# Kernel optimization log

Hardware: AMD Instinct MI355X
Metric: run time of the kernel (lower is better)

Reference implementation:

```python
import jax, jax.numpy as jnp
import numpy as np

SEQ_LEN = 4096
D_IN = 1024
D_OUT = 1024


def setup_inputs() -> dict:
    key = jax.random.key(0)
    k_x, k_q, k_k, k_v = jax.random.split(key, 4)
    s = 1.0 / np.sqrt(D_IN)
    return {
        "x": jax.random.normal(k_x, (SEQ_LEN, D_IN), dtype=jnp.float32),
        "W_query": jax.random.normal(k_q, (D_IN, D_OUT), dtype=jnp.float32) * s,
        "W_key": jax.random.normal(k_k, (D_IN, D_OUT), dtype=jnp.float32) * s,
        "W_value": jax.random.normal(k_v, (D_IN, D_OUT), dtype=jnp.float32) * s,
    }


def reference(x, W_query, W_key, W_value):
    # QKV projections (Linear without bias): [S, d_out]
    q = x @ W_query
    k = x @ W_key
    v = x @ W_value
    # Full S x S score matrix, causal mask, scaled softmax
    scores = q @ k.T  # [S, S]
    seq_len = x.shape[0]
    causal = jnp.tril(jnp.ones((seq_len, seq_len), dtype=bool))
    scores = jnp.where(causal, scores, -jnp.inf)
    scale = 1.0 / jnp.sqrt(jnp.asarray(k.shape[-1], dtype=scores.dtype))
    attn = jax.nn.softmax(scores * scale, axis=-1)
    return attn @ v  # [S, d_out]
```

## Files before the change

### kernel.cpp

```cpp
#include <hip/hip_runtime.h>
#include <math.h>

#define SEQ 4096
#define DIM 1024

typedef unsigned short u16;
typedef __attribute__((ext_vector_type(8))) short short8;
typedef __attribute__((ext_vector_type(4))) float floatx4;
typedef __attribute__((ext_vector_type(4))) unsigned short us4;

__device__ __forceinline__ float bf2f(u16 u) {
    union { unsigned int i; float f; } c; c.i = ((unsigned int)u) << 16; return c.f;
}
__device__ __forceinline__ u16 f2bf(float f) {
    union { float f; unsigned int i; } c; c.f = f;
    return (u16)((c.i + 0x7fffu + ((c.i >> 16) & 1u)) >> 16);
}
__device__ __forceinline__ void gload_lds16(const u16* g, u16* l) {
    __builtin_amdgcn_global_load_lds((const __attribute__((address_space(1))) void*)g,
                                     (__attribute__((address_space(3))) void*)l, 16, 0, 0);
}

__device__ __forceinline__ void pipe128(const u16* __restrict__ A,
                                        const u16* __restrict__ B,
                                        u16 (&As)[3][4096], u16 (&Bs)[3][4096],
                                        int lda, int ldb, int row0, int col0,
                                        int wave, int lane,
                                        floatx4 (&acc)[4][4]) {
    const int wm = wave & 1, wn = wave >> 1;
    const int s0 = wave * 128 + lane;
    const int s1 = s0 + 64;
    const int r0s = s0 >> 2, q0s = ((s0 & 3) ^ ((s0 >> 3) & 3)) * 8;
    const int r1s = s1 >> 2, q1s = ((s1 & 3) ^ ((s1 >> 3) & 3)) * 8;
    const u16* aP0 = A + (size_t)(row0 + r0s) * lda + q0s;
    const u16* aP1 = A + (size_t)(row0 + r1s) * lda + q1s;
    const u16* bP0 = B + (size_t)(col0 + r0s) * ldb + q0s;
    const u16* bP1 = B + (size_t)(col0 + r1s) * ldb + q1s;
    const int l0 = wave * 1024;
    const int frow = lane & 15;
    const int xq = (((lane >> 4) ^ ((frow >> 1) & 3))) * 8;

    auto stage = [&](int c) {
        gload_lds16(aP0, &As[c][l0]);
        gload_lds16(aP1, &As[c][l0 + 512]);
        gload_lds16(bP0, &Bs[c][l0]);
        gload_lds16(bP1, &Bs[c][l0 + 512]);
        aP0 += 32; aP1 += 32; bP0 += 32; bP1 += 32;
    };
    stage(0);
    stage(1);

    auto compute_tile = [&](int c) {
        short8 af[4], bfr[4];
#pragma unroll
        for (int t = 0; t < 4; ++t) {
            af[t]  = *(const short8*)&As[c][(wm * 64 + t * 16 + frow) * 32 + xq];
            bfr[t] = *(const short8*)&Bs[c][(wn * 64 + t * 16 + frow) * 32 + xq];
        }
#pragma unroll
        for (int mt = 0; mt < 4; ++mt)
#pragma unroll
            for (int nt = 0; nt < 4; ++nt)
                acc[mt][nt] = __builtin_amdgcn_mfma_f32_16x16x32_bf16(
                    af[mt], bfr[nt], acc[mt][nt], 0, 0, 0);
    };

    int cur = 0, pre = 2;
    for (int it = 0; it < 30; ++it) {
        asm volatile("s_waitcnt vmcnt(4)\n\ts_barrier" ::: "memory");
        short8 af[4], bfr[4];
#pragma unroll
        for (int t = 0; t < 4; ++t) {
            af[t]  = *(const short8*)&As[cur][(wm * 64 + t * 16 + frow) * 32 + xq];
            bfr[t] = *(const short8*)&Bs[cur][(wn * 64 + t * 16 + frow) * 32 + xq];
        }
        stage(pre);
#pragma unroll
        for (int mt = 0; mt < 4; ++mt)
#pragma unroll
            for (int nt = 0; nt < 4; ++nt)
                acc[mt][nt] = __builtin_amdgcn_mfma_f32_16x16x32_bf16(
                    af[mt], bfr[nt], acc[mt][nt], 0, 0, 0);
        cur = (cur == 2) ? 0 : cur + 1;
        pre = (pre == 2) ? 0 : pre + 1;
    }
    asm volatile("s_waitcnt vmcnt(4)\n\ts_barrier" ::: "memory");
    compute_tile(cur);
    cur = (cur == 2) ? 0 : cur + 1;
    asm volatile("s_waitcnt vmcnt(0)\n\ts_barrier" ::: "memory");
    compute_tile(cur);
}

__global__ __launch_bounds__(256) void projQK(const u16* __restrict__ xb,
                                              const u16* __restrict__ Wt,
                                              u16* __restrict__ QK,
                                              float scale0) {
    __shared__ u16 As[3][4096], Bs[3][4096];
    const int row0 = blockIdx.y * 128;
    const int col0 = blockIdx.x * 128;
    const int tid = threadIdx.x, wave = tid >> 6, lane = tid & 63;
    const int wm = wave & 1, wn = wave >> 1;

    floatx4 acc[4][4] = {};
    pipe128(xb, Wt, As, Bs, DIM, DIM, row0, col0, wave, lane, acc);

    const int cr = (lane >> 4) * 4, cc = lane & 15;
    const float sc = (col0 < 1024) ? scale0 : 1.0f;
#pragma unroll
    for (int mt = 0; mt < 4; ++mt)
#pragma unroll
        for (int nt = 0; nt < 4; ++nt)
#pragma unroll
            for (int r = 0; r < 4; ++r) {
                const int row = row0 + wm * 64 + mt * 16 + cr + r;
                const int col = col0 + wn * 64 + nt * 16 + cc;
                QK[(size_t)row * 2048 + col] = f2bf(acc[mt][nt][r] * sc);
            }
}

__global__ __launch_bounds__(256) void scoresV(const u16* __restrict__ QK,
                                               const u16* __restrict__ xb,
                                               const u16* __restrict__ Wt,
                                               u16* __restrict__ E,
                                               u16* __restrict__ Vt,
                                               float* __restrict__ Lsum) {
    __shared__ u16 As[3][4096], Bs[3][4096];
    const int t = blockIdx.x;
    const int tid = threadIdx.x, wave = tid >> 6, lane = tid & 63;
    const int wm = wave & 1, wn = wave >> 1;
    const int cr = (lane >> 4) * 4, cc = lane & 15;

    floatx4 acc[4][4] = {};
    if (t < 256) {
        const int row0 = (t >> 3) * 128;
        const int colv = (t & 7) * 128;
        pipe128(xb, Wt, As, Bs, DIM, DIM, row0, 2048 + colv, wave, lane, acc);
#pragma unroll
        for (int mt = 0; mt < 4; ++mt)
#pragma unroll
            for (int nt = 0; nt < 4; ++nt) {
                const int row = row0 + wm * 64 + mt * 16 + cr;
                const int col = colv + wn * 64 + nt * 16 + cc;
                us4 o = { f2bf(acc[mt][nt][0]), f2bf(acc[mt][nt][1]),
                          f2bf(acc[mt][nt][2]), f2bf(acc[mt][nt][3]) };
                *(us4*)&Vt[(size_t)col * SEQ + row] = o;
            }
    } else {
        const int s = t - 256;
        int by = (int)((sqrtf(8.0f * s + 1.0f) - 1.0f) * 0.5f);
        while ((by + 1) * (by + 2) / 2 <= s) ++by;
        while (by * (by + 1) / 2 > s) --by;
        const int bx = s - by * (by + 1) / 2;
        const int row0 = by * 128, col0 = bx * 128;
        pipe128(QK, QK + 1024, As, Bs, 2048, 2048, row0, col0, wave, lane, acc);
#pragma unroll
        for (int mt = 0; mt < 4; ++mt) {
#pragma unroll
            for (int r = 0; r < 4; ++r) {
                const int grow = row0 + wm * 64 + mt * 16 + cr + r;
                float rowsum = 0.f;
#pragma unroll
                for (int nt = 0; nt < 4; ++nt) {
                    const int gcol = col0 + wn * 64 + nt * 16 + cc;
                    const float e = (gcol <= grow) ? __expf(acc[mt][nt][r]) : 0.f;
                    rowsum += e;
                    E[(size_t)grow * SEQ + gcol] = f2bf(e);
                }
                rowsum += __shfl_xor(rowsum, 1);
                rowsum += __shfl_xor(rowsum, 2);
                rowsum += __shfl_xor(rowsum, 4);
                rowsum += __shfl_xor(rowsum, 8);
                if (cc == 0) atomicAdd(&Lsum[grow], rowsum);
            }
        }
    }
}

__global__ __launch_bounds__(256) void pv64(const u16* __restrict__ E,
                                            const u16* __restrict__ Vt,
                                            float* __restrict__ O,
                                            const float* __restrict__ Lsum) {
    const int lin = blockIdx.x + (blockIdx.y << 4);
    const int c = lin & 7;
    const int j = lin >> 3;
    const int x = j & 15;
    const int m = j >> 4;
    const unsigned long long PK = 0x2F3F20301F0F1000ULL;
    const int base = (int)((PK >> (m * 8)) & 0x3F);
    const int r = base + ((m & 2) ? -c : c);
    const int row0 = r * 64;
    const int col0 = x * 64;
    const int kend = row0 + 64;

    __shared__ u16 As[3][2048], Bs[3][2048];

    const int tid  = threadIdx.x;
    const int wave = tid >> 6;
    const int lane = tid & 63;
    const int wm = wave & 1;
    const int wn = wave >> 1;

    const int s0 = wave * 64 + lane;
    const int r0 = s0 >> 2, q0 = ((s0 & 3) ^ ((s0 >> 3) & 3)) * 8;
    const u16* aP = E  + (size_t)(row0 + r0) * SEQ + q0;
    const u16* bP = Vt + (size_t)(col0 + r0) * SEQ + q0;
    const int l0 = wave * 512;

    floatx4 acc[2][2] = {};
    const int niter = kend >> 5;
    const int frow = lane & 15;
    const int xq = (((lane >> 4) ^ ((frow >> 1) & 3))) * 8;
    const int mrow0 = wm * 32, nrow0 = wn * 32;

    auto stage = [&](int cb) {
        gload_lds16(aP, &As[cb][l0]);
        gload_lds16(bP, &Bs[cb][l0]);
        aP += 32; bP += 32;
    };
    stage(0);
    stage(1);

    auto compute_tile = [&](int cb) {
        short8 af[2], bfr[2];
#pragma unroll
        for (int t = 0; t < 2; ++t) {
            af[t]  = *(const short8*)&As[cb][(mrow0 + t * 16 + frow) * 32 + xq];
            bfr[t] = *(const short8*)&Bs[cb][(nrow0 + t * 16 + frow) * 32 + xq];
        }
#pragma unroll
        for (int mt = 0; mt < 2; ++mt)
#pragma unroll
            for (int nt = 0; nt < 2; ++nt)
                acc[mt][nt] = __builtin_amdgcn_mfma_f32_16x16x32_bf16(
                    af[mt], bfr[nt], acc[mt][nt], 0, 0, 0);
    };

    int cur = 0, pre = 2;
    for (int it = 0; it < niter - 2; ++it) {
        asm volatile("s_waitcnt vmcnt(2)\n\ts_barrier" ::: "memory");
        short8 af[2], bfr[2];
#pragma unroll
        for (int t = 0; t < 2; ++t) {
            af[t]  = *(const short8*)&As[cur][(mrow0 + t * 16 + frow) * 32 + xq];
            bfr[t] = *(const short8*)&Bs[cur][(nrow0 + t * 16 + frow) * 32 + xq];
        }
        stage(pre);
#pragma unroll
        for (int mt = 0; mt < 2; ++mt)
#pragma unroll
            for (int nt = 0; nt < 2; ++nt)
                acc[mt][nt] = __builtin_amdgcn_mfma_f32_16x16x32_bf16(
                    af[mt], bfr[nt], acc[mt][nt], 0, 0, 0);
        cur = (cur == 2) ? 0 : cur + 1;
        pre = (pre == 2) ? 0 : pre + 1;
    }
    asm volatile("s_waitcnt vmcnt(2)\n\ts_barrier" ::: "memory");
    compute_tile(cur);
    cur = (cur == 2) ? 0 : cur + 1;
    asm volatile("s_waitcnt vmcnt(0)\n\ts_barrier" ::: "memory");
    compute_tile(cur);

    float* Oo = O;
    const int cr = (lane >> 4) * 4, cc = lane & 15;
#pragma unroll
    for (int mt = 0; mt < 2; ++mt)
#pragma unroll
        for (int rr = 0; rr < 4; ++rr) {
            const int grow = row0 + wm * 32 + mt * 16 + cr + rr;
            const float invl = __builtin_amdgcn_rcpf(Lsum[grow]);
#pragma unroll
            for (int nt = 0; nt < 2; ++nt) {
                const int col = col0 + wn * 32 + nt * 16 + cc;
                Oo[(size_t)grow * DIM + col] = acc[mt][nt][rr] * invl;
            }
        }
}

__global__ __launch_bounds__(256) void prep(const float* __restrict__ x,
                                            const float* __restrict__ W0,
                                            const float* __restrict__ W1,
                                            const float* __restrict__ W2,
                                            u16* __restrict__ xb,
                                            u16* __restrict__ Wt,
                                            float* __restrict__ Lsum) {
    __shared__ float tile[32][33];
    const int b = blockIdx.x;
    const int tid = threadIdx.x;
    if (b < 4096) {
        const size_t i = ((size_t)b * 256 + tid) * 4;
        const float4 v = *(const float4*)(x + i);
        us4 o = { f2bf(v.x), f2bf(v.y), f2bf(v.z), f2bf(v.w) };
        *(us4*)(xb + i) = o;
    } else if (b < 7168) {
        const int t = b - 4096;
        const int z = t >> 10;
        const int idx = t & 1023;
        const float* W = (z == 0) ? W0 : (z == 1) ? W1 : W2;
        u16* out = Wt + (size_t)z * DIM * DIM;
        const int bx = (idx & 31) * 32;
        const int by = (idx >> 5) * 32;
        const int tx = tid & 31;
        const int ty = (tid >> 5) * 4;
#pragma unroll
        for (int r = 0; r < 4; ++r)
            tile[ty + r][tx] = W[(size_t)(by + ty + r) * DIM + bx + tx];
        __syncthreads();
#pragma unroll
        for (int r = 0; r < 4; ++r)
            out[(size_t)(bx + ty + r) * DIM + by + tx] = f2bf(tile[tx][ty + r]);
    } else {
        const int t = b - 7168;
        *(float4*)(Lsum + (size_t)(t * 256 + tid) * 4) =
            make_float4(0.f, 0.f, 0.f, 0.f);
    }
}

extern "C" void kernel_launch(void* const* d_in, const int* in_sizes, int n_in,
                              void* d_out, int out_size, void* d_ws, size_t ws_size,
                              hipStream_t stream) {
    const float* x  = (const float*)d_in[0];
    const float* Wq = (const float*)d_in[1];
    const float* Wk = (const float*)d_in[2];
    const float* Wv = (const float*)d_in[3];

    u16* xb    = (u16*)d_ws;
    u16* Wt    = xb  + (size_t)SEQ * DIM;
    u16* QK    = Wt  + (size_t)3072 * DIM;
    u16* Vt    = QK  + (size_t)SEQ * 2048;
    u16* E     = Vt  + (size_t)DIM * SEQ;
    float* Lsum = (float*)(E + (size_t)SEQ * SEQ);

    prep<<<7172, 256, 0, stream>>>(x, Wq, Wk, Wv, xb, Wt, Lsum);

    projQK<<<dim3(16, 32), 256, 0, stream>>>(xb, Wt, QK, 0.03125f);

    scoresV<<<784, 256, 0, stream>>>(QK, xb, Wt, E, Vt, Lsum);

    pv64<<<dim3(16, 64), 256, 0, stream>>>(E, Vt, (float*)d_out, Lsum);
}
```

Before: 192.2 us.

## Switch GEMM pipelines to double-buffered LDS and fold V projection into QK GEMM

The shared pipeline and the PV kernel now use two LDS buffers instead of three. Each iteration adds an lgkmcnt wait and a barrier, then issues the next prefetch into the buffer that was just read. The V projection moves out of the scores kernel into a single QKV projection launch, and scores becomes its own causal-tile kernel. The smaller LDS footprint may raise occupancy and give a more even grid split, but the extra barrier per k-step can expose load latency.

```diff
diff --git a/kernel.cpp b/kernel.cpp
--- a/kernel.cpp
+++ b/kernel.cpp
@@ -23,7 +23,7 @@
 
 __device__ __forceinline__ void pipe128(const u16* __restrict__ A,
                                         const u16* __restrict__ B,
-                                        u16 (&As)[3][4096], u16 (&Bs)[3][4096],
+                                        u16 (&As)[2][4096], u16 (&Bs)[2][4096],
                                         int lda, int ldb, int row0, int col0,
                                         int wave, int lane,
                                         floatx4 (&acc)[4][4]) {
@@ -50,52 +50,53 @@
     stage(0);
     stage(1);
 
-    auto compute_tile = [&](int c) {
+    int cur = 0;
+    for (int it = 0; it < 30; ++it) {
+        asm volatile("s_waitcnt vmcnt(4)\n\ts_barrier" ::: "memory");
         short8 af[4], bfr[4];
 #pragma unroll
         for (int t = 0; t < 4; ++t) {
-            af[t]  = *(const short8*)&As[c][(wm * 64 + t * 16 + frow) * 32 + xq];
-            bfr[t] = *(const short8*)&Bs[c][(wn * 64 + t * 16 + frow) * 32 + xq];
-        }
+            af[t]  = *(const short8*)&As[cur][(wm * 64 + t * 16 + frow) * 32 + xq];
+            bfr[t] = *(const short8*)&Bs[cur][(wn * 64 + t * 16 + frow) * 32 + xq];
+        }
+        asm volatile("s_waitcnt lgkmcnt(0)\n\ts_barrier" ::: "memory");
+        stage(cur);
 #pragma unroll
         for (int mt = 0; mt < 4; ++mt)
 #pragma unroll
             for (int nt = 0; nt < 4; ++nt)
                 acc[mt][nt] = __builtin_amdgcn_mfma_f32_16x16x32_bf16(
                     af[mt], bfr[nt], acc[mt][nt], 0, 0, 0);
-    };
-
-    int cur = 0, pre = 2;
-    for (int it = 0; it < 30; ++it) {
-        asm volatile("s_waitcnt vmcnt(4)\n\ts_barrier" ::: "memory");
+        cur ^= 1;
+    }
+#pragma unroll
+    for (int fin = 0; fin < 2; ++fin) {
+        if (fin == 0)
+            asm volatile("s_waitcnt vmcnt(4)\n\ts_barrier" ::: "memory");
+        else
+            asm volatile("s_waitcnt vmcnt(0)\n\ts_barrier" ::: "memory");
         short8 af[4], bfr[4];
 #pragma unroll
         for (int t = 0; t < 4; ++t) {
             af[t]  = *(const short8*)&As[cur][(wm * 64 + t * 16 + frow) * 32 + xq];
             bfr[t] = *(const short8*)&Bs[cur][(wn * 64 + t * 16 + frow) * 32 + xq];
         }
-        stage(pre);
 #pragma unroll
         for (int mt = 0; mt < 4; ++mt)
 #pragma unroll
             for (int nt = 0; nt < 4; ++nt)
                 acc[mt][nt] = __builtin_amdgcn_mfma_f32_16x16x32_bf16(
                     af[mt], bfr[nt], acc[mt][nt], 0, 0, 0);
-        cur = (cur == 2) ? 0 : cur + 1;
-        pre = (pre == 2) ? 0 : pre + 1;
-    }
-    asm volatile("s_waitcnt vmcnt(4)\n\ts_barrier" ::: "memory");
-    compute_tile(cur);
-    cur = (cur == 2) ? 0 : cur + 1;
-    asm volatile("s_waitcnt vmcnt(0)\n\ts_barrier" ::: "memory");
-    compute_tile(cur);
-}
-
-__global__ __launch_bounds__(256) void projQK(const u16* __restrict__ xb,
-                                              const u16* __restrict__ Wt,
-                                              u16* __restrict__ QK,
-                                              float scale0) {
-    __shared__ u16 As[3][4096], Bs[3][4096];
+        cur ^= 1;
+    }
+}
+
+__global__ __launch_bounds__(256) void gemm128(const u16* __restrict__ xb,
+                                               const u16* __restrict__ Wt,
+                                               u16* __restrict__ QK,
+                                               u16* __restrict__ Vt,
+                                               float scale0) {
+    __shared__ u16 As[2][4096], Bs[2][4096];
     const int row0 = blockIdx.y * 128;
     const int col0 = blockIdx.x * 128;
     const int tid = threadIdx.x, wave = tid >> 6, lane = tid & 63;
@@ -105,73 +106,67 @@
     pipe128(xb, Wt, As, Bs, DIM, DIM, row0, col0, wave, lane, acc);
 
     const int cr = (lane >> 4) * 4, cc = lane & 15;
-    const float sc = (col0 < 1024) ? scale0 : 1.0f;
-#pragma unroll
-    for (int mt = 0; mt < 4; ++mt)
-#pragma unroll
-        for (int nt = 0; nt < 4; ++nt)
-#pragma unroll
-            for (int r = 0; r < 4; ++r) {
-                const int row = row0 + wm * 64 + mt * 16 + cr + r;
-                const int col = col0 + wn * 64 + nt * 16 + cc;
-                QK[(size_t)row * 2048 + col] = f2bf(acc[mt][nt][r] * sc);
-            }
-}
-
-__global__ __launch_bounds__(256) void scoresV(const u16* __restrict__ QK,
-                                               const u16* __restrict__ xb,
-                                               const u16* __restrict__ Wt,
-                                               u16* __restrict__ E,
-                                               u16* __restrict__ Vt,
-                                               float* __restrict__ Lsum) {
-    __shared__ u16 As[3][4096], Bs[3][4096];
-    const int t = blockIdx.x;
-    const int tid = threadIdx.x, wave = tid >> 6, lane = tid & 63;
-    const int wm = wave & 1, wn = wave >> 1;
-    const int cr = (lane >> 4) * 4, cc = lane & 15;
-
-    floatx4 acc[4][4] = {};
-    if (t < 256) {
-        const int row0 = (t >> 3) * 128;
-        const int colv = (t & 7) * 128;
-        pipe128(xb, Wt, As, Bs, DIM, DIM, row0, 2048 + colv, wave, lane, acc);
+    if (col0 >= 2048) {
 #pragma unroll
         for (int mt = 0; mt < 4; ++mt)
 #pragma unroll
             for (int nt = 0; nt < 4; ++nt) {
                 const int row = row0 + wm * 64 + mt * 16 + cr;
-                const int col = colv + wn * 64 + nt * 16 + cc;
+                const int col = (col0 - 2048) + wn * 64 + nt * 16 + cc;
                 us4 o = { f2bf(acc[mt][nt][0]), f2bf(acc[mt][nt][1]),
                           f2bf(acc[mt][nt][2]), f2bf(acc[mt][nt][3]) };
                 *(us4*)&Vt[(size_t)col * SEQ + row] = o;
             }
     } else {
-        const int s = t - 256;
-        int by = (int)((sqrtf(8.0f * s + 1.0f) - 1.0f) * 0.5f);
-        while ((by + 1) * (by + 2) / 2 <= s) ++by;
-        while (by * (by + 1) / 2 > s) --by;
-        const int bx = s - by * (by + 1) / 2;
-        const int row0 = by * 128, col0 = bx * 128;
-        pipe128(QK, QK + 1024, As, Bs, 2048, 2048, row0, col0, wave, lane, acc);
-#pragma unroll
-        for (int mt = 0; mt < 4; ++mt) {
-#pragma unroll
-            for (int r = 0; r < 4; ++r) {
-                const int grow = row0 + wm * 64 + mt * 16 + cr + r;
-                float rowsum = 0.f;
-#pragma unroll
-                for (int nt = 0; nt < 4; ++nt) {
-                    const int gcol = col0 + wn * 64 + nt * 16 + cc;
-                    const float e = (gcol <= grow) ? __expf(acc[mt][nt][r]) : 0.f;
-                    rowsum += e;
-                    E[(size_t)grow * SEQ + gcol] = f2bf(e);
+        const float sc = (col0 < 1024) ? scale0 : 1.0f;
+#pragma unroll
+        for (int mt = 0; mt < 4; ++mt)
+#pragma unroll
+            for (int nt = 0; nt < 4; ++nt)
+#pragma unroll
+                for (int r = 0; r < 4; ++r) {
+                    const int row = row0 + wm * 64 + mt * 16 + cr + r;
+                    const int col = col0 + wn * 64 + nt * 16 + cc;
+                    QK[(size_t)row * 2048 + col] = f2bf(acc[mt][nt][r] * sc);
                 }
-                rowsum += __shfl_xor(rowsum, 1);
-                rowsum += __shfl_xor(rowsum, 2);
-                rowsum += __shfl_xor(rowsum, 4);
-                rowsum += __shfl_xor(rowsum, 8);
-                if (cc == 0) atomicAdd(&Lsum[grow], rowsum);
+    }
+}
+
+__global__ __launch_bounds__(256) void scores(const u16* __restrict__ QK,
+                                              u16* __restrict__ E,
+                                              float* __restrict__ Lsum) {
+    __shared__ u16 As[2][4096], Bs[2][4096];
+    const int t = blockIdx.x;
+    int by = (int)((sqrtf(8.0f * t + 1.0f) - 1.0f) * 0.5f);
+    while ((by + 1) * (by + 2) / 2 <= t) ++by;
+    while (by * (by + 1) / 2 > t) --by;
+    const int bx = t - by * (by + 1) / 2;
+    const int row0 = by * 128, col0 = bx * 128;
+    const int tid = threadIdx.x, wave = tid >> 6, lane = tid & 63;
+    const int wm = wave & 1, wn = wave >> 1;
+
+    floatx4 acc[4][4] = {};
+    pipe128(QK, QK + 1024, As, Bs, 2048, 2048, row0, col0, wave, lane, acc);
+
+    const int cr = (lane >> 4) * 4, cc = lane & 15;
+#pragma unroll
+    for (int mt = 0; mt < 4; ++mt) {
+#pragma unroll
+        for (int r = 0; r < 4; ++r) {
+            const int grow = row0 + wm * 64 + mt * 16 + cr + r;
+            float rowsum = 0.f;
+#pragma unroll
+            for (int nt = 0; nt < 4; ++nt) {
+                const int gcol = col0 + wn * 64 + nt * 16 + cc;
+                const float e = (gcol <= grow) ? __expf(acc[mt][nt][r]) : 0.f;
+                rowsum += e;
+                E[(size_t)grow * SEQ + gcol] = f2bf(e);
             }
+            rowsum += __shfl_xor(rowsum, 1);
+            rowsum += __shfl_xor(rowsum, 2);
+            rowsum += __shfl_xor(rowsum, 4);
+            rowsum += __shfl_xor(rowsum, 8);
+            if (cc == 0) atomicAdd(&Lsum[grow], rowsum);
         }
     }
 }
@@ -192,7 +187,7 @@
     const int col0 = x * 64;
     const int kend = row0 + 64;
 
-    __shared__ u16 As[3][2048], Bs[3][2048];
+    __shared__ u16 As[2][2048], Bs[2][2048];
 
     const int tid  = threadIdx.x;
     const int wave = tid >> 6;
@@ -220,47 +215,46 @@
     stage(0);
     stage(1);
 
-    auto compute_tile = [&](int cb) {
+    int cur = 0;
+    for (int it = 0; it < niter - 2; ++it) {
+        asm volatile("s_waitcnt vmcnt(2)\n\ts_barrier" ::: "memory");
         short8 af[2], bfr[2];
 #pragma unroll
         for (int t = 0; t < 2; ++t) {
-            af[t]  = *(const short8*)&As[cb][(mrow0 + t * 16 + frow) * 32 + xq];
-            bfr[t] = *(const short8*)&Bs[cb][(nrow0 + t * 16 + frow) * 32 + xq];
-        }
+            af[t]  = *(const short8*)&As[cur][(mrow0 + t * 16 + frow) * 32 + xq];
+            bfr[t] = *(const short8*)&Bs[cur][(nrow0 + t * 16 + frow) * 32 + xq];
+        }
+        asm volatile("s_waitcnt lgkmcnt(0)\n\ts_barrier" ::: "memory");
+        stage(cur);
 #pragma unroll
         for (int mt = 0; mt < 2; ++mt)
 #pragma unroll
             for (int nt = 0; nt < 2; ++nt)
                 acc[mt][nt] = __builtin_amdgcn_mfma_f32_16x16x32_bf16(
                     af[mt], bfr[nt], acc[mt][nt], 0, 0, 0);
-    };
-
-    int cur = 0, pre = 2;
-    for (int it = 0; it < niter - 2; ++it) {
-        asm volatile("s_waitcnt vmcnt(2)\n\ts_barrier" ::: "memory");
+        cur ^= 1;
+    }
+#pragma unroll
+    for (int fin = 0; fin < 2; ++fin) {
+        if (fin == 0)
+            asm volatile("s_waitcnt vmcnt(2)\n\ts_barrier" ::: "memory");
+        else
+            asm volatile("s_waitcnt vmcnt(0)\n\ts_barrier" ::: "memory");
         short8 af[2], bfr[2];
 #pragma unroll
         for (int t = 0; t < 2; ++t) {
             af[t]  = *(const short8*)&As[cur][(mrow0 + t * 16 + frow) * 32 + xq];
             bfr[t] = *(const short8*)&Bs[cur][(nrow0 + t * 16 + frow) * 32 + xq];
         }
-        stage(pre);
 #pragma unroll
         for (int mt = 0; mt < 2; ++mt)
 #pragma unroll
             for (int nt = 0; nt < 2; ++nt)
                 acc[mt][nt] = __builtin_amdgcn_mfma_f32_16x16x32_bf16(
                     af[mt], bfr[nt], acc[mt][nt], 0, 0, 0);
-        cur = (cur == 2) ? 0 : cur + 1;
-        pre = (pre == 2) ? 0 : pre + 1;
-    }
-    asm volatile("s_waitcnt vmcnt(2)\n\ts_barrier" ::: "memory");
-    compute_tile(cur);
-    cur = (cur == 2) ? 0 : cur + 1;
-    asm volatile("s_waitcnt vmcnt(0)\n\ts_barrier" ::: "memory");
-    compute_tile(cur);
-
-    float* Oo = O;
+        cur ^= 1;
+    }
+
     const int cr = (lane >> 4) * 4, cc = lane & 15;
 #pragma unroll
     for (int mt = 0; mt < 2; ++mt)
@@ -271,7 +265,7 @@
 #pragma unroll
             for (int nt = 0; nt < 2; ++nt) {
                 const int col = col0 + wn * 32 + nt * 16 + cc;
-                Oo[(size_t)grow * DIM + col] = acc[mt][nt][rr] * invl;
+                O[(size_t)grow * DIM + col] = acc[mt][nt][rr] * invl;
             }
         }
 }
@@ -332,9 +326,9 @@
 
     prep<<<7172, 256, 0, stream>>>(x, Wq, Wk, Wv, xb, Wt, Lsum);
 
-    projQK<<<dim3(16, 32), 256, 0, stream>>>(xb, Wt, QK, 0.03125f);
-
-    scoresV<<<784, 256, 0, stream>>>(QK, xb, Wt, E, Vt, Lsum);
+    gemm128<<<dim3(24, 32), 256, 0, stream>>>(xb, Wt, QK, Vt, 0.03125f);
+
+    scores<<<528, 256, 0, stream>>>(QK, E, Lsum);
 
     pv64<<<dim3(16, 64), 256, 0, stream>>>(E, Vt, (float*)d_out, Lsum);
 }
```

New measurement: 209.8 us. 1.09x slower.

## Use 256x128 tiles with 512 threads and move V projection into projection kernel

Applied to the files above, without the earlier changes.

Replaces the 128x128, 256-thread GEMM pipeline with a 256x128 tile handled by 8 waves and a double-buffered loop that uses __syncthreads instead of a triple-buffered vmcnt pipeline. The V projection moves out of the scores kernel into a single projection launch covering Q, K and V. The scores launch now enumerates 272 causal 256x128 blocks. Larger tiles increase operand reuse per block but cut the number of blocks and the depth of prefetch, which may leave compute units idle or expose load latency.

```diff
diff --git a/kernel.cpp b/kernel.cpp
--- a/kernel.cpp
+++ b/kernel.cpp
@@ -21,41 +21,43 @@
                                      (__attribute__((address_space(3))) void*)l, 16, 0, 0);
 }
 
-__device__ __forceinline__ void pipe128(const u16* __restrict__ A,
+__device__ __forceinline__ void pipe256(const u16* __restrict__ A,
                                         const u16* __restrict__ B,
-                                        u16 (&As)[3][4096], u16 (&Bs)[3][4096],
+                                        u16 (&As)[2][8192], u16 (&Bs)[2][4096],
                                         int lda, int ldb, int row0, int col0,
                                         int wave, int lane,
                                         floatx4 (&acc)[4][4]) {
-    const int wm = wave & 1, wn = wave >> 1;
-    const int s0 = wave * 128 + lane;
-    const int s1 = s0 + 64;
-    const int r0s = s0 >> 2, q0s = ((s0 & 3) ^ ((s0 >> 3) & 3)) * 8;
-    const int r1s = s1 >> 2, q1s = ((s1 & 3) ^ ((s1 >> 3) & 3)) * 8;
-    const u16* aP0 = A + (size_t)(row0 + r0s) * lda + q0s;
-    const u16* aP1 = A + (size_t)(row0 + r1s) * lda + q1s;
-    const u16* bP0 = B + (size_t)(col0 + r0s) * ldb + q0s;
-    const u16* bP1 = B + (size_t)(col0 + r1s) * ldb + q1s;
-    const int l0 = wave * 1024;
+    const int wm = wave & 3, wn = wave >> 2;
+    const int sa0 = wave * 128 + lane, sa1 = sa0 + 64;
+    const int ra0 = sa0 >> 2, qa0 = ((sa0 & 3) ^ ((sa0 >> 3) & 3)) * 8;
+    const int ra1 = sa1 >> 2, qa1 = ((sa1 & 3) ^ ((sa1 >> 3) & 3)) * 8;
+    const int sb0 = wave * 64 + lane;
+    const int rb0 = sb0 >> 2, qb0 = ((sb0 & 3) ^ ((sb0 >> 3) & 3)) * 8;
+    const u16* aP0 = A + (size_t)(row0 + ra0) * lda + qa0;
+    const u16* aP1 = A + (size_t)(row0 + ra1) * lda + qa1;
+    const u16* bP0 = B + (size_t)(col0 + rb0) * ldb + qb0;
+    const int lA = wave * 1024;
+    const int lB = wave * 512;
     const int frow = lane & 15;
     const int xq = (((lane >> 4) ^ ((frow >> 1) & 3))) * 8;
 
     auto stage = [&](int c) {
-        gload_lds16(aP0, &As[c][l0]);
-        gload_lds16(aP1, &As[c][l0 + 512]);
-        gload_lds16(bP0, &Bs[c][l0]);
-        gload_lds16(bP1, &Bs[c][l0 + 512]);
-        aP0 += 32; aP1 += 32; bP0 += 32; bP1 += 32;
+        gload_lds16(aP0, &As[c][lA]);
+        gload_lds16(aP1, &As[c][lA + 512]);
+        gload_lds16(bP0, &Bs[c][lB]);
+        aP0 += 32; aP1 += 32; bP0 += 32;
     };
+
     stage(0);
-    stage(1);
-
-    auto compute_tile = [&](int c) {
+    __syncthreads();
+    for (int it = 0; it < 32; ++it) {
+        const int cur = it & 1;
+        if (it < 31) stage(cur ^ 1);
         short8 af[4], bfr[4];
 #pragma unroll
         for (int t = 0; t < 4; ++t) {
-            af[t]  = *(const short8*)&As[c][(wm * 64 + t * 16 + frow) * 32 + xq];
-            bfr[t] = *(const short8*)&Bs[c][(wn * 64 + t * 16 + frow) * 32 + xq];
+            af[t]  = *(const short8*)&As[cur][(wm * 64 + t * 16 + frow) * 32 + xq];
+            bfr[t] = *(const short8*)&Bs[cur][(wn * 64 + t * 16 + frow) * 32 + xq];
         }
 #pragma unroll
         for (int mt = 0; mt < 4; ++mt)
@@ -63,115 +65,86 @@
             for (int nt = 0; nt < 4; ++nt)
                 acc[mt][nt] = __builtin_amdgcn_mfma_f32_16x16x32_bf16(
                     af[mt], bfr[nt], acc[mt][nt], 0, 0, 0);
-    };
-
-    int cur = 0, pre = 2;
-    for (int it = 0; it < 30; ++it) {
-        asm volatile("s_waitcnt vmcnt(4)\n\ts_barrier" ::: "memory");
-        short8 af[4], bfr[4];
-#pragma unroll
-        for (int t = 0; t < 4; ++t) {
-            af[t]  = *(const short8*)&As[cur][(wm * 64 + t * 16 + frow) * 32 + xq];
-            bfr[t] = *(const short8*)&Bs[cur][(wn * 64 + t * 16 + frow) * 32 + xq];
-        }
-        stage(pre);
-#pragma unroll
-        for (int mt = 0; mt < 4; ++mt)
-#pragma unroll
-            for (int nt = 0; nt < 4; ++nt)
-                acc[mt][nt] = __builtin_amdgcn_mfma_f32_16x16x32_bf16(
-                    af[mt], bfr[nt], acc[mt][nt], 0, 0, 0);
-        cur = (cur == 2) ? 0 : cur + 1;
-        pre = (pre == 2) ? 0 : pre + 1;
-    }
-    asm volatile("s_waitcnt vmcnt(4)\n\ts_barrier" ::: "memory");
-    compute_tile(cur);
-    cur = (cur == 2) ? 0 : cur + 1;
-    asm volatile("s_waitcnt vmcnt(0)\n\ts_barrier" ::: "memory");
-    compute_tile(cur);
-}
-
-__global__ __launch_bounds__(256) void projQK(const u16* __restrict__ xb,
-                                              const u16* __restrict__ Wt,
-                                              u16* __restrict__ QK,
-                                              float scale0) {
-    __shared__ u16 As[3][4096], Bs[3][4096];
-    const int row0 = blockIdx.y * 128;
+        __syncthreads();
+    }
+}
+
+__global__ __launch_bounds__(512) void proj256(const u16* __restrict__ xb,
+                                               const u16* __restrict__ Wt,
+                                               u16* __restrict__ QK,
+                                               u16* __restrict__ Vt,
+                                               float scale0) {
+    __shared__ u16 As[2][8192], Bs[2][4096];
+    const int row0 = blockIdx.y * 256;
     const int col0 = blockIdx.x * 128;
     const int tid = threadIdx.x, wave = tid >> 6, lane = tid & 63;
-    const int wm = wave & 1, wn = wave >> 1;
+    const int wm = wave & 3, wn = wave >> 2;
 
     floatx4 acc[4][4] = {};
-    pipe128(xb, Wt, As, Bs, DIM, DIM, row0, col0, wave, lane, acc);
+    pipe256(xb, Wt, As, Bs, DIM, DIM, row0, col0, wave, lane, acc);
 
     const int cr = (lane >> 4) * 4, cc = lane & 15;
-    const float sc = (col0 < 1024) ? scale0 : 1.0f;
-#pragma unroll
-    for (int mt = 0; mt < 4; ++mt)
-#pragma unroll
-        for (int nt = 0; nt < 4; ++nt)
-#pragma unroll
-            for (int r = 0; r < 4; ++r) {
-                const int row = row0 + wm * 64 + mt * 16 + cr + r;
-                const int col = col0 + wn * 64 + nt * 16 + cc;
-                QK[(size_t)row * 2048 + col] = f2bf(acc[mt][nt][r] * sc);
-            }
-}
-
-__global__ __launch_bounds__(256) void scoresV(const u16* __restrict__ QK,
-                                               const u16* __restrict__ xb,
-                                               const u16* __restrict__ Wt,
-                                               u16* __restrict__ E,
-                                               u16* __restrict__ Vt,
-                                               float* __restrict__ Lsum) {
-    __shared__ u16 As[3][4096], Bs[3][4096];
-    const int t = blockIdx.x;
-    const int tid = threadIdx.x, wave = tid >> 6, lane = tid & 63;
-    const int wm = wave & 1, wn = wave >> 1;
-    const int cr = (lane >> 4) * 4, cc = lane & 15;
-
-    floatx4 acc[4][4] = {};
-    if (t < 256) {
-        const int row0 = (t >> 3) * 128;
-        const int colv = (t & 7) * 128;
-        pipe128(xb, Wt, As, Bs, DIM, DIM, row0, 2048 + colv, wave, lane, acc);
+    if (col0 >= 2048) {
 #pragma unroll
         for (int mt = 0; mt < 4; ++mt)
 #pragma unroll
             for (int nt = 0; nt < 4; ++nt) {
                 const int row = row0 + wm * 64 + mt * 16 + cr;
-                const int col = colv + wn * 64 + nt * 16 + cc;
+                const int col = (col0 - 2048) + wn * 64 + nt * 16 + cc;
                 us4 o = { f2bf(acc[mt][nt][0]), f2bf(acc[mt][nt][1]),
                           f2bf(acc[mt][nt][2]), f2bf(acc[mt][nt][3]) };
                 *(us4*)&Vt[(size_t)col * SEQ + row] = o;
             }
     } else {
-        const int s = t - 256;
-        int by = (int)((sqrtf(8.0f * s + 1.0f) - 1.0f) * 0.5f);
-        while ((by + 1) * (by + 2) / 2 <= s) ++by;
-        while (by * (by + 1) / 2 > s) --by;
-        const int bx = s - by * (by + 1) / 2;
-        const int row0 = by * 128, col0 = bx * 128;
-        pipe128(QK, QK + 1024, As, Bs, 2048, 2048, row0, col0, wave, lane, acc);
-#pragma unroll
-        for (int mt = 0; mt < 4; ++mt) {
-#pragma unroll
-            for (int r = 0; r < 4; ++r) {
-                const int grow = row0 + wm * 64 + mt * 16 + cr + r;
-                float rowsum = 0.f;
-#pragma unroll
-                for (int nt = 0; nt < 4; ++nt) {
-                    const int gcol = col0 + wn * 64 + nt * 16 + cc;
-                    const float e = (gcol <= grow) ? __expf(acc[mt][nt][r]) : 0.f;
-                    rowsum += e;
-                    E[(size_t)grow * SEQ + gcol] = f2bf(e);
+        const float sc = (col0 < 1024) ? scale0 : 1.0f;
+#pragma unroll
+        for (int mt = 0; mt < 4; ++mt)
+#pragma unroll
+            for (int nt = 0; nt < 4; ++nt)
+#pragma unroll
+                for (int r = 0; r < 4; ++r) {
+                    const int row = row0 + wm * 64 + mt * 16 + cr + r;
+                    const int col = col0 + wn * 64 + nt * 16 + cc;
+                    QK[(size_t)row * 2048 + col] = f2bf(acc[mt][nt][r] * sc);
                 }
-                rowsum += __shfl_xor(rowsum, 1);
-                rowsum += __shfl_xor(rowsum, 2);
-                rowsum += __shfl_xor(rowsum, 4);
-                rowsum += __shfl_xor(rowsum, 8);
-                if (cc == 0) atomicAdd(&Lsum[grow], rowsum);
+    }
+}
+
+__global__ __launch_bounds__(512) void scores256(const u16* __restrict__ QK,
+                                                 u16* __restrict__ E,
+                                                 float* __restrict__ Lsum) {
+    __shared__ u16 As[2][8192], Bs[2][4096];
+    const int t = blockIdx.x;
+    int R = (int)((sqrtf(4.0f * t + 1.0f) - 1.0f) * 0.5f);
+    while ((R + 1) * (R + 2) + R + 1 - 1 < t + 1) ++R;
+    while (R * R + R > t) --R;
+    const int bx = t - (R * R + R);
+    const int row0 = R * 256, col0 = bx * 128;
+    const int tid = threadIdx.x, wave = tid >> 6, lane = tid & 63;
+    const int wm = wave & 3, wn = wave >> 2;
+
+    floatx4 acc[4][4] = {};
+    pipe256(QK, QK + 1024, As, Bs, 2048, 2048, row0, col0, wave, lane, acc);
+
+    const int cr = (lane >> 4) * 4, cc = lane & 15;
+#pragma unroll
+    for (int mt = 0; mt < 4; ++mt) {
+#pragma unroll
+        for (int r = 0; r < 4; ++r) {
+            const int grow = row0 + wm * 64 + mt * 16 + cr + r;
+            float rowsum = 0.f;
+#pragma unroll
+            for (int nt = 0; nt < 4; ++nt) {
+                const int gcol = col0 + wn * 64 + nt * 16 + cc;
+                const float e = (gcol <= grow) ? __expf(acc[mt][nt][r]) : 0.f;
+                rowsum += e;
+                E[(size_t)grow * SEQ + gcol] = f2bf(e);
             }
+            rowsum += __shfl_xor(rowsum, 1);
+            rowsum += __shfl_xor(rowsum, 2);
+            rowsum += __shfl_xor(rowsum, 4);
+            rowsum += __shfl_xor(rowsum, 8);
+            if (cc == 0) atomicAdd(&Lsum[grow], rowsum);
         }
     }
 }
@@ -260,7 +233,6 @@
     asm volatile("s_waitcnt vmcnt(0)\n\ts_barrier" ::: "memory");
     compute_tile(cur);
 
-    float* Oo = O;
     const int cr = (lane >> 4) * 4, cc = lane & 15;
 #pragma unroll
     for (int mt = 0; mt < 2; ++mt)
@@ -271,7 +243,7 @@
 #pragma unroll
             for (int nt = 0; nt < 2; ++nt) {
                 const int col = col0 + wn * 32 + nt * 16 + cc;
-                Oo[(size_t)grow * DIM + col] = acc[mt][nt][rr] * invl;
+                O[(size_t)grow * DIM + col] = acc[mt][nt][rr] * invl;
             }
         }
 }
@@ -332,9 +304,9 @@
 
     prep<<<7172, 256, 0, stream>>>(x, Wq, Wk, Wv, xb, Wt, Lsum);
 
-    projQK<<<dim3(16, 32), 256, 0, stream>>>(xb, Wt, QK, 0.03125f);
-
-    scoresV<<<784, 256, 0, stream>>>(QK, xb, Wt, E, Vt, Lsum);
+    proj256<<<dim3(24, 16), 512, 0, stream>>>(xb, Wt, QK, Vt, 0.03125f);
+
+    scores256<<<272, 512, 0, stream>>>(QK, E, Lsum);
 
     pv64<<<dim3(16, 64), 256, 0, stream>>>(E, Vt, (float*)d_out, Lsum);
 }
```

Result: no change. 189.3 us (-1.5%).

## Rebalance QKV and score GEMMs into two 512-block launches with wide tiles

Applied to the files above, without the earlier changes.

The projection GEMM now computes K and V together in 128x256 wide tiles, with Q in 128x128 tiles, and V moves out of the scores kernel into the first launch. The score kernel now handles the causal triangle with 512 blocks: 16 wide tiles cover the last two diagonal-adjacent 128-blocks of the lower rows, and the rest are regular tiles. The aim is to balance work so each launch is exactly 512 blocks and to reuse the A tile across more output columns. The cost is a larger LDS footprint (Bs doubled) and more accumulator registers in the wide path, which may lower occupancy.

```diff
diff --git a/kernel.cpp b/kernel.cpp
--- a/kernel.cpp
+++ b/kernel.cpp
@@ -21,157 +21,262 @@
                                      (__attribute__((address_space(3))) void*)l, 16, 0, 0);
 }
 
-__device__ __forceinline__ void pipe128(const u16* __restrict__ A,
-                                        const u16* __restrict__ B,
-                                        u16 (&As)[3][4096], u16 (&Bs)[3][4096],
-                                        int lda, int ldb, int row0, int col0,
-                                        int wave, int lane,
-                                        floatx4 (&acc)[4][4]) {
+template <int MODE>
+__global__ __launch_bounds__(256) void qgemm(const u16* __restrict__ A,
+                                             const u16* __restrict__ B,
+                                             u16* __restrict__ Cout,
+                                             u16* __restrict__ VtOut,
+                                             float* __restrict__ Lsum,
+                                             int lda, int ldb, int ldc,
+                                             float scale0) {
+    __shared__ u16 As[3][4096];
+    __shared__ u16 Bs[3][8192];
+    const int tid = threadIdx.x, wave = tid >> 6, lane = tid & 63;
     const int wm = wave & 1, wn = wave >> 1;
-    const int s0 = wave * 128 + lane;
-    const int s1 = s0 + 64;
-    const int r0s = s0 >> 2, q0s = ((s0 & 3) ^ ((s0 >> 3) & 3)) * 8;
-    const int r1s = s1 >> 2, q1s = ((s1 & 3) ^ ((s1 >> 3) & 3)) * 8;
-    const u16* aP0 = A + (size_t)(row0 + r0s) * lda + q0s;
-    const u16* aP1 = A + (size_t)(row0 + r1s) * lda + q1s;
-    const u16* bP0 = B + (size_t)(col0 + r0s) * ldb + q0s;
-    const u16* bP1 = B + (size_t)(col0 + r1s) * ldb + q1s;
-    const int l0 = wave * 1024;
+
+    int row0, col0;
+    bool wide;
+    if (MODE == 0) {
+        const int t = blockIdx.x;
+        if (t < 256) { wide = true;  row0 = (t >> 3) * 128; col0 = 1024 + (t & 7) * 256; }
+        else { const int s = t - 256; wide = false; row0 = (s >> 3) * 128; col0 = (s & 7) * 128; }
+    } else {
+        const int t = blockIdx.x;
+        if (t < 16) { wide = true; const int R = 16 + t; row0 = R * 128; col0 = (R - 1) * 128; }
+        else {
+            wide = false;
+            const int s = t - 16;
+            int by, bx;
+            if (s < 136) {
+                by = (int)((sqrtf(8.0f * s + 1.0f) - 1.0f) * 0.5f);
+                while ((by + 1) * (by + 2) / 2 <= s) ++by;
+                while (by * (by + 1) / 2 > s) --by;
+                bx = s - by * (by + 1) / 2;
+            } else {
+                int u = s - 136;
+                by = 16;
+                while (u >= by - 1) { u -= by - 1; ++by; }
+                bx = u;
+            }
+            row0 = by * 128;
+            col0 = bx * 128;
+        }
+    }
+
     const int frow = lane & 15;
     const int xq = (((lane >> 4) ^ ((frow >> 1) & 3))) * 8;
-
-    auto stage = [&](int c) {
-        gload_lds16(aP0, &As[c][l0]);
-        gload_lds16(aP1, &As[c][l0 + 512]);
-        gload_lds16(bP0, &Bs[c][l0]);
-        gload_lds16(bP1, &Bs[c][l0 + 512]);
-        aP0 += 32; aP1 += 32; bP0 += 32; bP1 += 32;
-    };
-    stage(0);
-    stage(1);
-
-    auto compute_tile = [&](int c) {
-        short8 af[4], bfr[4];
-#pragma unroll
-        for (int t = 0; t < 4; ++t) {
-            af[t]  = *(const short8*)&As[c][(wm * 64 + t * 16 + frow) * 32 + xq];
-            bfr[t] = *(const short8*)&Bs[c][(wn * 64 + t * 16 + frow) * 32 + xq];
-        }
-#pragma unroll
-        for (int mt = 0; mt < 4; ++mt)
-#pragma unroll
-            for (int nt = 0; nt < 4; ++nt)
-                acc[mt][nt] = __builtin_amdgcn_mfma_f32_16x16x32_bf16(
-                    af[mt], bfr[nt], acc[mt][nt], 0, 0, 0);
-    };
-
-    int cur = 0, pre = 2;
-    for (int it = 0; it < 30; ++it) {
+    const int l0 = wave * 1024;
+    const int cr = (lane >> 4) * 4, cc = lane & 15;
+
+    const int sA0 = wave * 128 + lane, sA1 = sA0 + 64;
+    const int rA0 = sA0 >> 2, qA0 = ((sA0 & 3) ^ ((sA0 >> 3) & 3)) * 8;
+    const int rA1 = sA1 >> 2, qA1 = ((sA1 & 3) ^ ((sA1 >> 3) & 3)) * 8;
+    const u16* aP0 = A + (size_t)(row0 + rA0) * lda + qA0;
+    const u16* aP1 = A + (size_t)(row0 + rA1) * lda + qA1;
+
+    if (wide) {
+        const int sW0 = wave * 256 + lane;
+        const int sW1 = sW0 + 64, sW2 = sW0 + 128, sW3 = sW0 + 192;
+        const int rW0 = sW0 >> 2, qW0 = ((sW0 & 3) ^ ((sW0 >> 3) & 3)) * 8;
+        const int rW1 = sW1 >> 2, qW1 = ((sW1 & 3) ^ ((sW1 >> 3) & 3)) * 8;
+        const int rW2 = sW2 >> 2, qW2 = ((sW2 & 3) ^ ((sW2 >> 3) & 3)) * 8;
+        const int rW3 = sW3 >> 2, qW3 = ((sW3 & 3) ^ ((sW3 >> 3) & 3)) * 8;
+        const u16* bP0 = B + (size_t)(col0 + rW0) * ldb + qW0;
+        const u16* bP1 = B + (size_t)(col0 + rW1) * ldb + qW1;
+        const u16* bP2 = B + (size_t)(col0 + rW2) * ldb + qW2;
+        const u16* bP3 = B + (size_t)(col0 + rW3) * ldb + qW3;
+        const int lB = wave * 2048;
+
+        floatx4 acc[4][8] = {};
+        auto stage = [&](int c_) {
+            gload_lds16(aP0, &As[c_][l0]);
+            gload_lds16(aP1, &As[c_][l0 + 512]);
+            gload_lds16(bP0, &Bs[c_][lB]);
+            gload_lds16(bP1, &Bs[c_][lB + 512]);
+            gload_lds16(bP2, &Bs[c_][lB + 1024]);
+            gload_lds16(bP3, &Bs[c_][lB + 1536]);
+            aP0 += 32; aP1 += 32; bP0 += 32; bP1 += 32; bP2 += 32; bP3 += 32;
+        };
+        stage(0);
+        stage(1);
+
+        auto compute_tile = [&](int c_) {
+            short8 af[4], bfr[8];
+#pragma unroll
+            for (int t = 0; t < 4; ++t)
+                af[t] = *(const short8*)&As[c_][(wm * 64 + t * 16 + frow) * 32 + xq];
+#pragma unroll
+            for (int t = 0; t < 8; ++t)
+                bfr[t] = *(const short8*)&Bs[c_][(wn * 128 + t * 16 + frow) * 32 + xq];
+#pragma unroll
+            for (int mt = 0; mt < 4; ++mt)
+#pragma unroll
+                for (int nt = 0; nt < 8; ++nt)
+                    acc[mt][nt] = __builtin_amdgcn_mfma_f32_16x16x32_bf16(
+                        af[mt], bfr[nt], acc[mt][nt], 0, 0, 0);
+        };
+
+        int cur = 0, pre = 2;
+        for (int it = 0; it < 30; ++it) {
+            asm volatile("s_waitcnt vmcnt(6)\n\ts_barrier" ::: "memory");
+            short8 af[4], bfr[8];
+#pragma unroll
+            for (int t = 0; t < 4; ++t)
+                af[t] = *(const short8*)&As[cur][(wm * 64 + t * 16 + frow) * 32 + xq];
+#pragma unroll
+            for (int t = 0; t < 8; ++t)
+                bfr[t] = *(const short8*)&Bs[cur][(wn * 128 + t * 16 + frow) * 32 + xq];
+            stage(pre);
+#pragma unroll
+            for (int mt = 0; mt < 4; ++mt)
+#pragma unroll
+                for (int nt = 0; nt < 8; ++nt)
+                    acc[mt][nt] = __builtin_amdgcn_mfma_f32_16x16x32_bf16(
+                        af[mt], bfr[nt], acc[mt][nt], 0, 0, 0);
+            cur = (cur == 2) ? 0 : cur + 1;
+            pre = (pre == 2) ? 0 : pre + 1;
+        }
+        asm volatile("s_waitcnt vmcnt(6)\n\ts_barrier" ::: "memory");
+        compute_tile(cur);
+        cur = (cur == 2) ? 0 : cur + 1;
+        asm volatile("s_waitcnt vmcnt(0)\n\ts_barrier" ::: "memory");
+        compute_tile(cur);
+
+        if (MODE == 1) {
+#pragma unroll
+            for (int mt = 0; mt < 4; ++mt) {
+#pragma unroll
+                for (int r = 0; r < 4; ++r) {
+                    const int grow = row0 + wm * 64 + mt * 16 + cr + r;
+                    float rowsum = 0.f;
+#pragma unroll
+                    for (int nt = 0; nt < 8; ++nt) {
+                        const int gcol = col0 + wn * 128 + nt * 16 + cc;
+                        const float e = (gcol <= grow) ? __expf(acc[mt][nt][r]) : 0.f;
+                        rowsum += e;
+                        Cout[(size_t)grow * ldc + gcol] = f2bf(e);
+                    }
+                    rowsum += __shfl_xor(rowsum, 1);
+                    rowsum += __shfl_xor(rowsum, 2);
+                    rowsum += __shfl_xor(rowsum, 4);
+                    rowsum += __shfl_xor(rowsum, 8);
+                    if (cc == 0) atomicAdd(&Lsum[grow], rowsum);
+                }
+            }
+        } else if (col0 >= 2048) {
+#pragma unroll
+            for (int mt = 0; mt < 4; ++mt)
+#pragma unroll
+                for (int nt = 0; nt < 8; ++nt) {
+                    const int row = row0 + wm * 64 + mt * 16 + cr;
+                    const int col = (col0 - 2048) + wn * 128 + nt * 16 + cc;
+                    us4 o = { f2bf(acc[mt][nt][0]), f2bf(acc[mt][nt][1]),
+                              f2bf(acc[mt][nt][2]), f2bf(acc[mt][nt][3]) };
+                    *(us4*)&VtOut[(size_t)col * SEQ + row] = o;
+                }
+        } else {
+#pragma unroll
+            for (int mt = 0; mt < 4; ++mt)
+#pragma unroll
+                for (int nt = 0; nt < 8; ++nt)
+#pragma unroll
+                    for (int r = 0; r < 4; ++r) {
+                        const int row = row0 + wm * 64 + mt * 16 + cr + r;
+                        const int col = col0 + wn * 128 + nt * 16 + cc;
+                        Cout[(size_t)row * ldc + col] = f2bf(acc[mt][nt][r]);
+                    }
+        }
+    } else {
+        const int sB0 = wave * 128 + lane, sB1 = sB0 + 64;
+        const int rB0 = sB0 >> 2, qB0 = ((sB0 & 3) ^ ((sB0 >> 3) & 3)) * 8;
+        const int rB1 = sB1 >> 2, qB1 = ((sB1 & 3) ^ ((sB1 >> 3) & 3)) * 8;
+        const u16* bP0 = B + (size_t)(col0 + rB0) * ldb + qB0;
+        const u16* bP1 = B + (size_t)(col0 + rB1) * ldb + qB1;
+
+        floatx4 acc[4][4] = {};
+        auto stage = [&](int c_) {
+            gload_lds16(aP0, &As[c_][l0]);
+            gload_lds16(aP1, &As[c_][l0 + 512]);
+            gload_lds16(bP0, &Bs[c_][l0]);
+            gload_lds16(bP1, &Bs[c_][l0 + 512]);
+            aP0 += 32; aP1 += 32; bP0 += 32; bP1 += 32;
+        };
+        stage(0);
+        stage(1);
+
+        auto compute_tile = [&](int c_) {
+            short8 af[4], bfr[4];
+#pragma unroll
+            for (int t = 0; t < 4; ++t) {
+                af[t]  = *(const short8*)&As[c_][(wm * 64 + t * 16 + frow) * 32 + xq];
+                bfr[t] = *(const short8*)&Bs[c_][(wn * 64 + t * 16 + frow) * 32 + xq];
+            }
+#pragma unroll
+            for (int mt = 0; mt < 4; ++mt)
+#pragma unroll
+                for (int nt = 0; nt < 4; ++nt)
+                    acc[mt][nt] = __builtin_amdgcn_mfma_f32_16x16x32_bf16(
+                        af[mt], bfr[nt], acc[mt][nt], 0, 0, 0);
+        };
+
+        int cur = 0, pre = 2;
+        for (int it = 0; it < 30; ++it) {
+            asm volatile("s_waitcnt vmcnt(4)\n\ts_barrier" ::: "memory");
+            short8 af[4], bfr[4];
+#pragma unroll
+            for (int t = 0; t < 4; ++t) {
+                af[t]  = *(const short8*)&As[cur][(wm * 64 + t * 16 + frow) * 32 + xq];
+                bfr[t] = *(const short8*)&Bs[cur][(wn * 64 + t * 16 + frow) * 32 + xq];
+            }
+            stage(pre);
+#pragma unroll
+            for (int mt = 0; mt < 4; ++mt)
+#pragma unroll
+                for (int nt = 0; nt < 4; ++nt)
+                    acc[mt][nt] = __builtin_amdgcn_mfma_f32_16x16x32_bf16(
+                        af[mt], bfr[nt], acc[mt][nt], 0, 0, 0);
+            cur = (cur == 2) ? 0 : cur + 1;
+            pre = (pre == 2) ? 0 : pre + 1;
+        }
         asm volatile("s_waitcnt vmcnt(4)\n\ts_barrier" ::: "memory");
-        short8 af[4], bfr[4];
-#pragma unroll
-        for (int t = 0; t < 4; ++t) {
-            af[t]  = *(const short8*)&As[cur][(wm * 64 + t * 16 + frow) * 32 + xq];
-            bfr[t] = *(const short8*)&Bs[cur][(wn * 64 + t * 16 + frow) * 32 + xq];
-        }
-        stage(pre);
-#pragma unroll
-        for (int mt = 0; mt < 4; ++mt)
-#pragma unroll
-            for (int nt = 0; nt < 4; ++nt)
-                acc[mt][nt] = __builtin_amdgcn_mfma_f32_16x16x32_bf16(
-                    af[mt], bfr[nt], acc[mt][nt], 0, 0, 0);
+        compute_tile(cur);
         cur = (cur == 2) ? 0 : cur + 1;
-        pre = (pre == 2) ? 0 : pre + 1;
-    }
-    asm volatile("s_waitcnt vmcnt(4)\n\ts_barrier" ::: "memory");
-    compute_tile(cur);
-    cur = (cur == 2) ? 0 : cur + 1;
-    asm volatile("s_waitcnt vmcnt(0)\n\ts_barrier" ::: "memory");
-    compute_tile(cur);
-}
-
-__global__ __launch_bounds__(256) void projQK(const u16* __restrict__ xb,
-                                              const u16* __restrict__ Wt,
-                                              u16* __restrict__ QK,
-                                              float scale0) {
-    __shared__ u16 As[3][4096], Bs[3][4096];
-    const int row0 = blockIdx.y * 128;
-    const int col0 = blockIdx.x * 128;
-    const int tid = threadIdx.x, wave = tid >> 6, lane = tid & 63;
-    const int wm = wave & 1, wn = wave >> 1;
-
-    floatx4 acc[4][4] = {};
-    pipe128(xb, Wt, As, Bs, DIM, DIM, row0, col0, wave, lane, acc);
-
-    const int cr = (lane >> 4) * 4, cc = lane & 15;
-    const float sc = (col0 < 1024) ? scale0 : 1.0f;
-#pragma unroll
-    for (int mt = 0; mt < 4; ++mt)
-#pragma unroll
-        for (int nt = 0; nt < 4; ++nt)
-#pragma unroll
-            for (int r = 0; r < 4; ++r) {
-                const int row = row0 + wm * 64 + mt * 16 + cr + r;
-                const int col = col0 + wn * 64 + nt * 16 + cc;
-                QK[(size_t)row * 2048 + col] = f2bf(acc[mt][nt][r] * sc);
-            }
-}
-
-__global__ __launch_bounds__(256) void scoresV(const u16* __restrict__ QK,
-                                               const u16* __restrict__ xb,
-                                               const u16* __restrict__ Wt,
-                                               u16* __restrict__ E,
-                                               u16* __restrict__ Vt,
-                                               float* __restrict__ Lsum) {
-    __shared__ u16 As[3][4096], Bs[3][4096];
-    const int t = blockIdx.x;
-    const int tid = threadIdx.x, wave = tid >> 6, lane = tid & 63;
-    const int wm = wave & 1, wn = wave >> 1;
-    const int cr = (lane >> 4) * 4, cc = lane & 15;
-
-    floatx4 acc[4][4] = {};
-    if (t < 256) {
-        const int row0 = (t >> 3) * 128;
-        const int colv = (t & 7) * 128;
-        pipe128(xb, Wt, As, Bs, DIM, DIM, row0, 2048 + colv, wave, lane, acc);
-#pragma unroll
-        for (int mt = 0; mt < 4; ++mt)
-#pragma unroll
-            for (int nt = 0; nt < 4; ++nt) {
-                const int row = row0 + wm * 64 + mt * 16 + cr;
-                const int col = colv + wn * 64 + nt * 16 + cc;
-                us4 o = { f2bf(acc[mt][nt][0]), f2bf(acc[mt][nt][1]),
-                          f2bf(acc[mt][nt][2]), f2bf(acc[mt][nt][3]) };
-                *(us4*)&Vt[(size_t)col * SEQ + row] = o;
-            }
-    } else {
-        const int s = t - 256;
-        int by = (int)((sqrtf(8.0f * s + 1.0f) - 1.0f) * 0.5f);
-        while ((by + 1) * (by + 2) / 2 <= s) ++by;
-        while (by * (by + 1) / 2 > s) --by;
-        const int bx = s - by * (by + 1) / 2;
-        const int row0 = by * 128, col0 = bx * 128;
-        pipe128(QK, QK + 1024, As, Bs, 2048, 2048, row0, col0, wave, lane, acc);
-#pragma unroll
-        for (int mt = 0; mt < 4; ++mt) {
-#pragma unroll
-            for (int r = 0; r < 4; ++r) {
-                const int grow = row0 + wm * 64 + mt * 16 + cr + r;
-                float rowsum = 0.f;
-#pragma unroll
-                for (int nt = 0; nt < 4; ++nt) {
-                    const int gcol = col0 + wn * 64 + nt * 16 + cc;
-                    const float e = (gcol <= grow) ? __expf(acc[mt][nt][r]) : 0.f;
-                    rowsum += e;
-                    E[(size_t)grow * SEQ + gcol] = f2bf(e);
+        asm volatile("s_waitcnt vmcnt(0)\n\ts_barrier" ::: "memory");
+        compute_tile(cur);
+
+        if (MODE == 1) {
+#pragma unroll
+            for (int mt = 0; mt < 4; ++mt) {
+#pragma unroll
+                for (int r = 0; r < 4; ++r) {
+                    const int grow = row0 + wm * 64 + mt * 16 + cr + r;
+                    float rowsum = 0.f;
+#pragma unroll
+                    for (int nt = 0; nt < 4; ++nt) {
+                        const int gcol = col0 + wn * 64 + nt * 16 + cc;
+                        const float e = (gcol <= grow) ? __expf(acc[mt][nt][r]) : 0.f;
+                        rowsum += e;
+                        Cout[(size_t)grow * ldc + gcol] = f2bf(e);
+                    }
+                    rowsum += __shfl_xor(rowsum, 1);
+                    rowsum += __shfl_xor(rowsum, 2);
+                    rowsum += __shfl_xor(rowsum, 4);
+                    rowsum += __shfl_xor(rowsum, 8);
+                    if (cc == 0) atomicAdd(&Lsum[grow], rowsum);
                 }
-                rowsum += __shfl_xor(rowsum, 1);
-                rowsum += __shfl_xor(rowsum, 2);
-                rowsum += __shfl_xor(rowsum, 4);
-                rowsum += __shfl_xor(rowsum, 8);
-                if (cc == 0) atomicAdd(&Lsum[grow], rowsum);
-            }
+            }
+        } else {
+            const float sc = (col0 < 1024) ? scale0 : 1.0f;
+#pragma unroll
+            for (int mt = 0; mt < 4; ++mt)
+#pragma unroll
+                for (int nt = 0; nt < 4; ++nt)
+#pragma unroll
+                    for (int r = 0; r < 4; ++r) {
+                        const int row = row0 + wm * 64 + mt * 16 + cr + r;
+                        const int col = col0 + wn * 64 + nt * 16 + cc;
+                        Cout[(size_t)row * ldc + col] = f2bf(acc[mt][nt][r] * sc);
+                    }
         }
     }
 }
@@ -260,7 +365,6 @@
     asm volatile("s_waitcnt vmcnt(0)\n\ts_barrier" ::: "memory");
     compute_tile(cur);
 
-    float* Oo = O;
     const int cr = (lane >> 4) * 4, cc = lane & 15;
 #pragma unroll
     for (int mt = 0; mt < 2; ++mt)
@@ -271,7 +375,7 @@
 #pragma unroll
             for (int nt = 0; nt < 2; ++nt) {
                 const int col = col0 + wn * 32 + nt * 16 + cc;
-                Oo[(size_t)grow * DIM + col] = acc[mt][nt][rr] * invl;
+                O[(size_t)grow * DIM + col] = acc[mt][nt][rr] * invl;
             }
         }
 }
@@ -332,9 +436,11 @@
 
     prep<<<7172, 256, 0, stream>>>(x, Wq, Wk, Wv, xb, Wt, Lsum);
 
-    projQK<<<dim3(16, 32), 256, 0, stream>>>(xb, Wt, QK, 0.03125f);
-
-    scoresV<<<784, 256, 0, stream>>>(QK, xb, Wt, E, Vt, Lsum);
+    qgemm<0><<<512, 256, 0, stream>>>(xb, Wt, QK, Vt, nullptr,
+                                      DIM, DIM, 2048, 0.03125f);
+
+    qgemm<1><<<512, 256, 0, stream>>>(QK, QK + 1024, E, nullptr, Lsum,
+                                      2048, 2048, SEQ, 1.0f);
 
     pv64<<<dim3(16, 64), 256, 0, stream>>>(E, Vt, (float*)d_out, Lsum);
 }
```

Result: slower. 217.6 us (+13.2%).
